# Optimization experiments

Measured on AMD Instinct MI355X. Metric: run time of the kernel, lower is better.

The kernel has to match this reference:

```python
import jax, jax.numpy as jnp
import numpy as np

N_NODES = 100000
N_EDGES = 1600000


def setup_inputs() -> dict:
    key = jax.random.key(0)
    ks = jax.random.split(key, 12)
    s = lambda d: 1.0 / np.sqrt(d)
    inp = {
        "x": jax.random.normal(ks[0], (N_NODES, 64), dtype=jnp.float32),
        "edge_index": jax.random.randint(ks[1], (2, N_EDGES), 0, N_NODES, dtype=jnp.int64),
        "W_embed": jax.random.normal(ks[2], (64, 128), dtype=jnp.float32) * s(64),
        "eps1": jnp.zeros((), jnp.float32),
        "w1a": jax.random.normal(ks[3], (128, 128), dtype=jnp.float32) * s(128),
        "b1a": jnp.zeros((128,), jnp.float32),
        "w1b": jax.random.normal(ks[4], (128, 128), dtype=jnp.float32) * s(128),
        "b1b": jnp.zeros((128,), jnp.float32),
        "eps2": jnp.zeros((), jnp.float32),
        "w2a": jax.random.normal(ks[5], (128, 256), dtype=jnp.float32) * s(128),
        "b2a": jnp.zeros((256,), jnp.float32),
        "w2b": jax.random.normal(ks[6], (256, 128), dtype=jnp.float32) * s(256),
        "b2b": jnp.zeros((128,), jnp.float32),
        "eps3": jnp.zeros((), jnp.float32),
        "w3a": jax.random.normal(ks[7], (128, 256), dtype=jnp.float32) * s(128),
        "b3a": jnp.zeros((256,), jnp.float32),
        "w3b": jax.random.normal(ks[8], (256, 128), dtype=jnp.float32) * s(256),
        "b3b": jnp.zeros((128,), jnp.float32),
    }
    return inp


def _aggregate(h, src, dst, n):
    # GINConv sum aggregation: out[i] = sum_{(j,i) in E} h[j]
    return jax.ops.segment_sum(h[src], dst, num_segments=n)


def reference(x, edge_index, W_embed, eps1, w1a, b1a, w1b, b1b,
              eps2, w2a, b2a, w2b, b2b, eps3, w3a, b3a, w3b, b3b):
    src, dst = edge_index[0], edge_index[1]
    n = x.shape[0]
    # node_attr_encoder: linear embedding (dropout p=0 -> identity)
    h = x @ W_embed  # [N, dim]
    # conv1: nn((1+eps)*h + sum_neighbors), nn = Lin->ReLU->Lin
    z = (1.0 + eps1) * h + _aggregate(h, src, dst, n)
    h = jax.nn.relu(z @ w1a + b1a) @ w1b + b1b
    # conv2/conv3: nn = Lin->ReLU->Lin->ReLU
    z = (1.0 + eps2) * h + _aggregate(h, src, dst, n)
    h = jax.nn.relu(jax.nn.relu(z @ w2a + b2a) @ w2b + b2b)
    z = (1.0 + eps3) * h + _aggregate(h, src, dst, n)
    h = jax.nn.relu(jax.nn.relu(z @ w3a + b3a) @ w3b + b3b)
    return h
```

## Files before the change

kernel.cpp:

```cpp
#include <hip/hip_runtime.h>
#include <hip/hip_bf16.h>
#include <stdint.h>


typedef __attribute__((ext_vector_type(8))) short short8;
typedef __attribute__((ext_vector_type(16))) float float16v;

#define BKT 512
#define NBMAX 256

__device__ __forceinline__ float b2f_lo(unsigned int u) {
    return __uint_as_float(u << 16);
}
__device__ __forceinline__ float b2f_hi(unsigned int u) {
    return __uint_as_float(u & 0xffff0000u);
}
__device__ __forceinline__ unsigned short f2b(float f) {
    unsigned int u = __float_as_uint(f);
    return (unsigned short)((u + 0x7fffu + ((u >> 16) & 1u)) >> 16);
}

__global__ void detect_i64_kernel(const unsigned int* ei, int* flag) {
    if (threadIdx.x == 0) {
        int is64 = 1;
        for (int e = 0; e < 64; ++e)
            if (ei[2 * e + 1] != 0u) { is64 = 0; break; }
        *flag = is64;
    }
}

__device__ __forceinline__ int edge_at(const int* ei32, int is64, long long pos) {
    if (is64) return (int)(((const long long*)ei32)[pos]);
    return ei32[pos];
}

__global__ __launch_bounds__(256) void part_hist_kernel(
        const int* __restrict__ ei, const int* __restrict__ flag,
        int* __restrict__ bh, int E, int NB, int PB) {
    __shared__ int h[NBMAX];
    const int g = blockIdx.x, tid = threadIdx.x;
    const int is64 = *flag;
    for (int i = tid; i < NB; i += 256) h[i] = 0;
    __syncthreads();
    const int e0 = g * PB, e1 = min(e0 + PB, E);
    for (int e = e0 + tid; e < e1; e += 256) {
        int d = edge_at(ei, is64, (long long)E + e);
        atomicAdd(&h[d >> 9], 1);
    }
    __syncthreads();
    for (int i = tid; i < NB; i += 256) bh[i * gridDim.x + g] = h[i];
}

__global__ __launch_bounds__(1024) void scan1_kernel(
        const int* __restrict__ in, int* __restrict__ out,
        int* __restrict__ partial, int n) {
    __shared__ int sm[1024];
    const int t = threadIdx.x;
    const int i = blockIdx.x * 1024 + t;
    int v = (i < n) ? in[i] : 0;
    sm[t] = v;
    __syncthreads();
#pragma unroll
    for (int off = 1; off < 1024; off <<= 1) {
        int x = (t >= off) ? sm[t - off] : 0;
        __syncthreads();
        sm[t] += x;
        __syncthreads();
    }
    if (i < n) out[i] = sm[t] - v;
    if (t == 1023) partial[blockIdx.x] = sm[1023];
}

__global__ __launch_bounds__(256) void scan2_kernel(
        int* __restrict__ partial, int* __restrict__ blockoff, int g1) {
    __shared__ int sm[256];
    const int t = threadIdx.x;
    int v = (t < g1) ? partial[t] : 0;
    sm[t] = v;
    __syncthreads();
#pragma unroll
    for (int off = 1; off < 256; off <<= 1) {
        int x = (t >= off) ? sm[t - off] : 0;
        __syncthreads();
        sm[t] += x;
        __syncthreads();
    }
    blockoff[t] = sm[t] - v;
}

__global__ __launch_bounds__(1024) void scan3g_kernel(
        int* __restrict__ a, const int* __restrict__ blockoff, int n) {
    int i = blockIdx.x * 1024 + threadIdx.x;
    if (i < n) a[i] += blockoff[blockIdx.x];
}

__global__ __launch_bounds__(256) void part_scatter_kernel(
        const int* __restrict__ ei, const int* __restrict__ flag,
        const int* __restrict__ bhs, unsigned int* __restrict__ staged,
        int E, int NB, int PB) {
    __shared__ int cur[NBMAX];
    const int g = blockIdx.x, tid = threadIdx.x;
    const int is64 = *flag;
    for (int i = tid; i < NB; i += 256) cur[i] = bhs[i * gridDim.x + g];
    __syncthreads();
    const int e0 = g * PB, e1 = min(e0 + PB, E);
    for (int e = e0 + tid; e < e1; e += 256) {
        int d = edge_at(ei, is64, (long long)E + e);
        int s = edge_at(ei, is64, (long long)e);
        int b = d >> 9;
        int p = atomicAdd(&cur[b], 1);
        staged[p] = ((unsigned int)(d & (BKT - 1)) << 17) | (unsigned int)s;
    }
}

__global__ __launch_bounds__(256) void csr_local_kernel(
        const unsigned int* __restrict__ staged, const int* __restrict__ bhs,
        int* __restrict__ offs, int* __restrict__ csr, int N, int E, int NB, int G2) {
    __shared__ int hist[BKT];
    __shared__ int cur[BKT];
    const int b = blockIdx.x;
    const int tid = threadIdx.x;
    const int start = bhs[b * G2];
    const int end = (b + 1 < NB) ? bhs[(b + 1) * G2] : E;
    const int node0 = b * BKT;
    for (int i = tid; i < BKT; i += 256) hist[i] = 0;
    __syncthreads();
    for (int i = start + tid; i < end; i += 256)
        atomicAdd(&hist[staged[i] >> 17], 1);
    __syncthreads();
    const int i0 = tid * 2, i1 = i0 + 1;
    for (int off = 1; off < BKT; off <<= 1) {
        int v0 = (i0 >= off) ? hist[i0 - off] : 0;
        int v1 = (i1 >= off) ? hist[i1 - off] : 0;
        __syncthreads();
        hist[i0] += v0;
        hist[i1] += v1;
        __syncthreads();
    }
    for (int i = tid; i < BKT; i += 256) {
        int node = node0 + i;
        if (node < N) {
            int e0 = start + ((i == 0) ? 0 : hist[i - 1]);
            offs[node] = e0;
            cur[i] = e0;
        }
    }
    if (b == NB - 1 && tid == 0) offs[N] = E;
    __syncthreads();
    for (int i = start + tid; i < end; i += 256) {
        unsigned int v = staged[i];
        int dl = v >> 17;
        int src = (int)(v & 0x1ffff);
        int p = atomicAdd(&cur[dl], 1);
        csr[p] = src;
    }
}

struct PW { const float* W; unsigned short* o; int K; int KOUT; };
struct PWAll { PW d[7]; int cum[8]; };

__global__ __launch_bounds__(256) void packall_kernel(PWAll P) {
    int id = blockIdx.x * blockDim.x + threadIdx.x;
    if (id >= P.cum[7]) return;
    int w = 0;
#pragma unroll
    for (int k = 1; k < 7; ++k) w += (id >= P.cum[k]);
    const int local = id - P.cum[w];
    const float* W = P.d[w].W;
    unsigned short* out = P.d[w].o;
    const int K = P.d[w].K, KOUT = P.d[w].KOUT;
    const int KS = K / 16;
    const int l = local & 63;
    const int s = (local >> 6) % KS;
    const int T = local / (KS * 64);
    const int kbase = s * 16 + ((l >> 5) << 3);
    const int n = T * 32 + (l & 31);
#pragma unroll
    for (int j = 0; j < 8; ++j)
        out[(long long)local * 8 + j] = f2b(W[(long long)(kbase + j) * KOUT + n]);
}

__global__ __launch_bounds__(256) void mm_embed(
        const float* __restrict__ X, const unsigned short* __restrict__ Wp,
        unsigned short* __restrict__ out, int Mreal) {
    constexpr int KS = 4;
    const int tid = threadIdx.x;
    const int w = tid >> 6;
    const int l = tid & 63;
    const int lm = l & 31;
    const int lk = l >> 5;
    const int wr = w & 1, wc = w >> 1;
    const long long R0 = (long long)blockIdx.x * 128 + wr * 64;
    const int T0 = (wc * 64) >> 5;

    const long long r0 = (R0 + lm < Mreal) ? (R0 + lm) : (Mreal - 1);
    const long long r1 = (R0 + 32 + lm < Mreal) ? (R0 + 32 + lm) : (Mreal - 1);
    const float* xr0 = X + r0 * 64 + lk * 8;
    const float* xr1 = X + r1 * 64 + lk * 8;
    const unsigned short* bb0 = Wp + ((long long)T0 * KS * 64 + l) * 8;
    const unsigned short* bb1 = Wp + ((long long)(T0 + 1) * KS * 64 + l) * 8;

    float16v acc00 = {}, acc01 = {}, acc10 = {}, acc11 = {};
#pragma unroll
    for (int s = 0; s < KS; ++s) {
        float4 f0a = *(const float4*)(xr0 + s * 16);
        float4 f0b = *(const float4*)(xr0 + s * 16 + 4);
        float4 f1a = *(const float4*)(xr1 + s * 16);
        float4 f1b = *(const float4*)(xr1 + s * 16 + 4);
        short8 a0, a1;
        a0[0] = (short)f2b(f0a.x); a0[1] = (short)f2b(f0a.y);
        a0[2] = (short)f2b(f0a.z); a0[3] = (short)f2b(f0a.w);
        a0[4] = (short)f2b(f0b.x); a0[5] = (short)f2b(f0b.y);
        a0[6] = (short)f2b(f0b.z); a0[7] = (short)f2b(f0b.w);
        a1[0] = (short)f2b(f1a.x); a1[1] = (short)f2b(f1a.y);
        a1[2] = (short)f2b(f1a.z); a1[3] = (short)f2b(f1a.w);
        a1[4] = (short)f2b(f1b.x); a1[5] = (short)f2b(f1b.y);
        a1[6] = (short)f2b(f1b.z); a1[7] = (short)f2b(f1b.w);
        short8 b0 = *(const short8*)(bb0 + (long long)s * 64 * 8);
        short8 b1 = *(const short8*)(bb1 + (long long)s * 64 * 8);
        acc00 = __builtin_amdgcn_mfma_f32_32x32x16_bf16(a0, b0, acc00, 0, 0, 0);
        acc01 = __builtin_amdgcn_mfma_f32_32x32x16_bf16(a0, b1, acc01, 0, 0, 0);
        acc10 = __builtin_amdgcn_mfma_f32_32x32x16_bf16(a1, b0, acc10, 0, 0, 0);
        acc11 = __builtin_amdgcn_mfma_f32_32x32x16_bf16(a1, b1, acc11, 0, 0, 0);
    }
    auto st = [&](float16v acc, long long rb, int col) {
#pragma unroll
        for (int r = 0; r < 16; ++r) {
            long long row = rb + (r & 3) + 8 * (r >> 2);
            out[row * 128 + col] = f2b(acc[r]);
        }
    };
    const long long rbase = R0 + 4 * lk;
    st(acc00, rbase,      wc * 64 + lm);
    st(acc01, rbase,      wc * 64 + 32 + lm);
    st(acc10, rbase + 32, wc * 64 + lm);
    st(acc11, rbase + 32, wc * 64 + 32 + lm);
}

__global__ __launch_bounds__(256) void aggz_kernel(
        const unsigned short* __restrict__ H, const int* __restrict__ offs,
        const int* __restrict__ csr, const float* __restrict__ eps,
        unsigned short* __restrict__ Z, int n) {
    const int node = blockIdx.x * 16 + (threadIdx.x >> 4);
    const int c8 = (threadIdx.x & 15) << 3;
    if (node >= n) return;
    const int beg = offs[node];
    const int end = offs[node + 1];
    float a0 = 0.f, a1 = 0.f, a2 = 0.f, a3 = 0.f;
    float a4 = 0.f, a5 = 0.f, a6 = 0.f, a7 = 0.f;
    int i = beg;
    for (; i + 3 < end; i += 4) {
        const int j0 = csr[i], j1 = csr[i + 1], j2 = csr[i + 2], j3 = csr[i + 3];
        const uint4 u0 = *(const uint4*)(H + ((long long)j0 << 7) + c8);
        const uint4 u1 = *(const uint4*)(H + ((long long)j1 << 7) + c8);
        const uint4 u2 = *(const uint4*)(H + ((long long)j2 << 7) + c8);
        const uint4 u3 = *(const uint4*)(H + ((long long)j3 << 7) + c8);
        a0 += (b2f_lo(u0.x) + b2f_lo(u1.x)) + (b2f_lo(u2.x) + b2f_lo(u3.x));
        a1 += (b2f_hi(u0.x) + b2f_hi(u1.x)) + (b2f_hi(u2.x) + b2f_hi(u3.x));
        a2 += (b2f_lo(u0.y) + b2f_lo(u1.y)) + (b2f_lo(u2.y) + b2f_lo(u3.y));
        a3 += (b2f_hi(u0.y) + b2f_hi(u1.y)) + (b2f_hi(u2.y) + b2f_hi(u3.y));
        a4 += (b2f_lo(u0.z) + b2f_lo(u1.z)) + (b2f_lo(u2.z) + b2f_lo(u3.z));
        a5 += (b2f_hi(u0.z) + b2f_hi(u1.z)) + (b2f_hi(u2.z) + b2f_hi(u3.z));
        a6 += (b2f_lo(u0.w) + b2f_lo(u1.w)) + (b2f_lo(u2.w) + b2f_lo(u3.w));
        a7 += (b2f_hi(u0.w) + b2f_hi(u1.w)) + (b2f_hi(u2.w) + b2f_hi(u3.w));
    }
    for (; i < end; ++i) {
        const uint4 u0 = *(const uint4*)(H + ((long long)csr[i] << 7) + c8);
        a0 += b2f_lo(u0.x); a1 += b2f_hi(u0.x);
        a2 += b2f_lo(u0.y); a3 += b2f_hi(u0.y);
        a4 += b2f_lo(u0.z); a5 += b2f_hi(u0.z);
        a6 += b2f_lo(u0.w); a7 += b2f_hi(u0.w);
    }
    const uint4 uh = *(const uint4*)(H + ((long long)node << 7) + c8);
    const float e = 1.0f + eps[0];
    a0 = fmaf(e, b2f_lo(uh.x), a0); a1 = fmaf(e, b2f_hi(uh.x), a1);
    a2 = fmaf(e, b2f_lo(uh.y), a2); a3 = fmaf(e, b2f_hi(uh.y), a3);
    a4 = fmaf(e, b2f_lo(uh.z), a4); a5 = fmaf(e, b2f_hi(uh.z), a5);
    a6 = fmaf(e, b2f_lo(uh.w), a6); a7 = fmaf(e, b2f_hi(uh.w), a7);
    uint4 o;
    o.x = ((unsigned int)f2b(a1) << 16) | (unsigned int)f2b(a0);
    o.y = ((unsigned int)f2b(a3) << 16) | (unsigned int)f2b(a2);
    o.z = ((unsigned int)f2b(a5) << 16) | (unsigned int)f2b(a4);
    o.w = ((unsigned int)f2b(a7) << 16) | (unsigned int)f2b(a6);
    *(uint4*)(Z + ((long long)node << 7) + c8) = o;
}

template<int KMID, bool RELU2, bool OUTF32>
__global__ __launch_bounds__(512) void fused_mlp(
        const unsigned short* __restrict__ Zin,
        const unsigned short* __restrict__ Wap, const float* __restrict__ ba,
        const unsigned short* __restrict__ Wbp, const float* __restrict__ bb,
        void* __restrict__ outp, int Mreal, int ntiles) {
    __shared__ unsigned short lds[16384];
    const int tid = threadIdx.x;
    const int w = tid >> 6;
    const int l = tid & 63;
    const int lm = l & 31;
    const int lk = l >> 5;
    const int wr = w & 1;
    const int wc = w >> 1;
    constexpr int KS1 = 8;
    constexpr int KSB = KMID / 16;
    constexpr int NH = KMID / 128;

    for (int tile = blockIdx.x; tile < ntiles; tile += gridDim.x) {
        const long long R0 = (long long)tile * 128;
        const unsigned short* arow0 = Zin + (R0 + wr * 64 + lm) * 128 + lk * 8;
        const unsigned short* arow1 = arow0 + 32 * 128;

        float16v d0 = {}, d1 = {};

        for (int h = 0; h < NH; ++h) {
            __syncthreads();

            {
                float16v c0 = {}, c1 = {};
                const int T1 = h * 4 + wc;
                const unsigned short* bp = Wap + ((long long)T1 * KS1 * 64 + l) * 8;
#pragma unroll
                for (int s = 0; s < KS1; ++s) {
                    short8 a0 = *(const short8*)(arow0 + s * 16);
                    short8 a1 = *(const short8*)(arow1 + s * 16);
                    short8 b = *(const short8*)(bp + (long long)s * 64 * 8);
                    c0 = __builtin_amdgcn_mfma_f32_32x32x16_bf16(a0, b, c0, 0, 0, 0);
                    c1 = __builtin_amdgcn_mfma_f32_32x32x16_bf16(a1, b, c1, 0, 0, 0);
                }
                auto wT = [&](float16v acc, int rbase, int cl) {
                    const float bv = ba[h * 128 + cl];
                    const int secT = cl >> 3;
                    const int cj = cl & 7;
#pragma unroll
                    for (int r = 0; r < 16; ++r) {
                        float v = fmaxf(acc[r] + bv, 0.f);
                        const int row = rbase + (r & 3) + 8 * (r >> 2);
                        lds[(secT * 128 + (row ^ (secT & 7))) * 8 + cj] = f2b(v);
                    }
                };
                wT(c0, wr * 64 + 4 * lk,      wc * 32 + lm);
                wT(c1, wr * 64 + 32 + 4 * lk, wc * 32 + lm);
            }
            __syncthreads();

            {
                const unsigned short* bp = Wbp + ((long long)wc * KSB * 64 + l) * 8;
#pragma unroll
                for (int s = 0; s < 8; ++s) {
                    const int sec = s * 2 + lk;
                    short8 a0 = *(const short8*)&lds[(sec * 128 + ((wr * 64 + lm) ^ (sec & 7))) * 8];
                    short8 a1 = *(const short8*)&lds[(sec * 128 + ((wr * 64 + 32 + lm) ^ (sec & 7))) * 8];
                    short8 b = *(const short8*)(bp + (long long)(h * 8 + s) * 64 * 8);
                    d0 = __builtin_amdgcn_mfma_f32_32x32x16_bf16(a0, b, d0, 0, 0, 0);
                    d1 = __builtin_amdgcn_mfma_f32_32x32x16_bf16(a1, b, d1, 0, 0, 0);
                }
            }
        }

        auto st = [&](float16v acc, int rbase, int col) {
            const float bv = bb[col];
#pragma unroll
            for (int r = 0; r < 16; ++r) {
                float v = acc[r] + bv;
                if (RELU2) v = fmaxf(v, 0.f);
                const long long row = R0 + rbase + (r & 3) + 8 * (r >> 2);
                if (OUTF32) {
                    if (row < Mreal) ((float*)outp)[row * 128 + col] = v;
                } else {
                    ((unsigned short*)outp)[row * 128 + col] = f2b(v);
                }
            }
        };
        st(d0, wr * 64 + 4 * lk,      wc * 32 + lm);
        st(d1, wr * 64 + 32 + 4 * lk, wc * 32 + lm);
    }
}

extern "C" void kernel_launch(void* const* d_in, const int* in_sizes, int n_in,
                              void* d_out, int out_size, void* d_ws, size_t ws_size,
                              hipStream_t stream) {
    const float* x    = (const float*)d_in[0];
    const int*   ei   = (const int*)d_in[1];
    const float* Wemb = (const float*)d_in[2];
    const float* eps1 = (const float*)d_in[3];
    const float* w1a  = (const float*)d_in[4];
    const float* b1a  = (const float*)d_in[5];
    const float* w1b  = (const float*)d_in[6];
    const float* b1b  = (const float*)d_in[7];
    const float* eps2 = (const float*)d_in[8];
    const float* w2a  = (const float*)d_in[9];
    const float* b2a  = (const float*)d_in[10];
    const float* w2b  = (const float*)d_in[11];
    const float* b2b  = (const float*)d_in[12];
    const float* eps3 = (const float*)d_in[13];
    const float* w3a  = (const float*)d_in[14];
    const float* b3a  = (const float*)d_in[15];
    const float* w3b  = (const float*)d_in[16];
    const float* b3b  = (const float*)d_in[17];

    const int N = in_sizes[0] / 64;
    const int E = in_sizes[1] / 2;
    const int Mpad = ((N + 127) / 128) * 128;
    const int NB = (N + BKT - 1) / BKT;
    const int G2 = 1024;
    const int PB = (E + G2 - 1) / G2;
    const int BH = NB * G2;

    char* ws = (char*)d_ws;
    size_t off = 0;
    auto alloc = [&](size_t bytes) -> void* {
        void* p = ws + off;
        off = (off + bytes + 255) & ~(size_t)255;
        return p;
    };
    unsigned short* Ha  = (unsigned short*)alloc((size_t)Mpad * 128 * 2);
    unsigned short* Hb2 = (unsigned short*)alloc((size_t)Mpad * 128 * 2);
    unsigned short* Zb  = (unsigned short*)alloc((size_t)Mpad * 128 * 2);
    unsigned short* pWe = (unsigned short*)alloc((size_t)64 * 128 * 2);
    unsigned short* p1a = (unsigned short*)alloc((size_t)128 * 128 * 2);
    unsigned short* p1b = (unsigned short*)alloc((size_t)128 * 128 * 2);
    unsigned short* p2a = (unsigned short*)alloc((size_t)128 * 256 * 2);
    unsigned short* p2b = (unsigned short*)alloc((size_t)256 * 128 * 2);
    unsigned short* p3a = (unsigned short*)alloc((size_t)128 * 256 * 2);
    unsigned short* p3b = (unsigned short*)alloc((size_t)256 * 128 * 2);
    int* offs = (int*)alloc((size_t)(N + 1) * 4);
    int* csr  = (int*)alloc((size_t)E * 4);
    unsigned int* staged = (unsigned int*)alloc((size_t)E * 4);
    int* bh   = (int*)alloc((size_t)BH * 4);
    int* bhs  = (int*)alloc((size_t)BH * 4);
    int* part = (int*)alloc(1024);
    int* boff = (int*)alloc(1024);
    int* flag = (int*)alloc(256);

    detect_i64_kernel<<<1, 64, 0, stream>>>((const unsigned int*)ei, flag);
    part_hist_kernel<<<G2, 256, 0, stream>>>(ei, flag, bh, E, NB, PB);
    const int G1 = (BH + 1023) / 1024;
    scan1_kernel<<<G1, 1024, 0, stream>>>(bh, bhs, part, BH);
    scan2_kernel<<<1, 256, 0, stream>>>(part, boff, G1);
    scan3g_kernel<<<G1, 1024, 0, stream>>>(bhs, boff, BH);
    part_scatter_kernel<<<G2, 256, 0, stream>>>(ei, flag, bhs, staged, E, NB, PB);
    csr_local_kernel<<<NB, 256, 0, stream>>>(staged, bhs, offs, csr, N, E, NB, G2);

    {
        PWAll P;
        const PW descs[7] = {
            {Wemb, pWe, 64, 128}, {w1a, p1a, 128, 128}, {w1b, p1b, 128, 128},
            {w2a, p2a, 128, 256}, {w2b, p2b, 256, 128}, {w3a, p3a, 128, 256},
            {w3b, p3b, 256, 128}};
        int c = 0;
        for (int k = 0; k < 7; ++k) {
            P.d[k] = descs[k];
            P.cum[k] = c;
            c += (descs[k].KOUT / 32) * (descs[k].K / 16) * 64;
        }
        P.cum[7] = c;
        packall_kernel<<<(c + 255) / 256, 256, 0, stream>>>(P);
    }

    const int MMB = Mpad / 128;
    const int AGB = (N + 15) / 16;
    const int PGRID = 512;

    mm_embed<<<MMB, 256, 0, stream>>>(x, pWe, Ha, N);

    aggz_kernel<<<AGB, 256, 0, stream>>>(Ha, offs, csr, eps1, Zb, N);
    fused_mlp<128, false, false><<<PGRID, 512, 0, stream>>>(Zb, p1a, b1a, p1b, b1b, Hb2, N, MMB);

    aggz_kernel<<<AGB, 256, 0, stream>>>(Hb2, offs, csr, eps2, Zb, N);
    fused_mlp<256, true, false><<<PGRID, 512, 0, stream>>>(Zb, p2a, b2a, p2b, b2b, Ha, N, MMB);

    aggz_kernel<<<AGB, 256, 0, stream>>>(Ha, offs, csr, eps3, Zb, N);
    fused_mlp<256, true, true><<<PGRID, 512, 0, stream>>>(Zb, p3a, b3a, p3b, b3b, d_out, N, MMB);
}
```

Before: 490.3 us.

## Rewrite fused MLP as per-wave register-resident strips without LDS round-trip

Replaces the 128-row block-tiled fused MLP, which staged the hidden activations through LDS with barriers, with a kernel in which each wave owns a 32-node strip. The first GEMM is computed transposed (weights as the A operand, Z as B) so the accumulator can be converted to bf16 with v_cvt_pk_bf16_f32 and rearranged with v_permlane32_swap directly into A-operand registers for the second GEMM. This removes LDS traffic and __syncthreads, and folds the first bias into the accumulator initialisation. In exchange it uses many more registers (whole hidden row held in registers), re-reads weights from global or cache once per wave, and launches one block per four strips instead of a persistent grid.

```diff
diff --git a/kernel.cpp b/kernel.cpp
--- a/kernel.cpp
+++ b/kernel.cpp
@@ -5,9 +5,14 @@
 
 typedef __attribute__((ext_vector_type(8))) short short8;
 typedef __attribute__((ext_vector_type(16))) float float16v;
+typedef __attribute__((ext_vector_type(4))) unsigned int uint4v;
 
 #define BKT 512
 #define NBMAX 256
+
+#define MFMA32 __builtin_amdgcn_mfma_f32_32x32x16_bf16
+
+union U4S8 { uint4v u; short8 s; };
 
 __device__ __forceinline__ float b2f_lo(unsigned int u) {
     return __uint_as_float(u << 16);
@@ -18,6 +23,14 @@
 __device__ __forceinline__ unsigned short f2b(float f) {
     unsigned int u = __float_as_uint(f);
     return (unsigned short)((u + 0x7fffu + ((u >> 16) & 1u)) >> 16);
+}
+__device__ __forceinline__ unsigned cvtpk_bf16(float a, float b) {
+    unsigned r;
+    asm("v_cvt_pk_bf16_f32 %0, %1, %2" : "=v"(r) : "v"(a), "v"(b));
+    return r;
+}
+__device__ __forceinline__ void perm32swap(unsigned& a, unsigned& b) {
+    asm("v_permlane32_swap_b32 %0, %1" : "+v"(a), "+v"(b));
 }
 
 __global__ void detect_i64_kernel(const unsigned int* ei, int* flag) {
@@ -218,10 +231,10 @@
         a1[6] = (short)f2b(f1b.z); a1[7] = (short)f2b(f1b.w);
         short8 b0 = *(const short8*)(bb0 + (long long)s * 64 * 8);
         short8 b1 = *(const short8*)(bb1 + (long long)s * 64 * 8);
-        acc00 = __builtin_amdgcn_mfma_f32_32x32x16_bf16(a0, b0, acc00, 0, 0, 0);
-        acc01 = __builtin_amdgcn_mfma_f32_32x32x16_bf16(a0, b1, acc01, 0, 0, 0);
-        acc10 = __builtin_amdgcn_mfma_f32_32x32x16_bf16(a1, b0, acc10, 0, 0, 0);
-        acc11 = __builtin_amdgcn_mfma_f32_32x32x16_bf16(a1, b1, acc11, 0, 0, 0);
+        acc00 = MFMA32(a0, b0, acc00, 0, 0, 0);
+        acc01 = MFMA32(a0, b1, acc01, 0, 0, 0);
+        acc10 = MFMA32(a1, b0, acc10, 0, 0, 0);
+        acc11 = MFMA32(a1, b1, acc11, 0, 0, 0);
     }
     auto st = [&](float16v acc, long long rb, int col) {
 #pragma unroll
@@ -285,92 +298,105 @@
     *(uint4*)(Z + ((long long)node << 7) + c8) = o;
 }
 
+
+#define CVT_TO_PA(ACC, CBASE) do {                                     \
+        unsigned X1 = cvtpk_bf16((ACC)[0], (ACC)[1]);                  \
+        unsigned Y1 = cvtpk_bf16((ACC)[4], (ACC)[5]);                  \
+        unsigned X2 = cvtpk_bf16((ACC)[2], (ACC)[3]);                  \
+        unsigned Y2 = cvtpk_bf16((ACC)[6], (ACC)[7]);                  \
+        perm32swap(X1, Y1); perm32swap(X2, Y2);                        \
+        U4S8 u0; u0.u[0] = X1; u0.u[1] = X2; u0.u[2] = Y1; u0.u[3] = Y2; \
+        pa[(CBASE)] = u0.s;                                            \
+        unsigned X3 = cvtpk_bf16((ACC)[8], (ACC)[9]);                  \
+        unsigned Y3 = cvtpk_bf16((ACC)[12], (ACC)[13]);                \
+        unsigned X4 = cvtpk_bf16((ACC)[10], (ACC)[11]);                \
+        unsigned Y4 = cvtpk_bf16((ACC)[14], (ACC)[15]);                \
+        perm32swap(X3, Y3); perm32swap(X4, Y4);                        \
+        U4S8 u1; u1.u[0] = X3; u1.u[1] = X4; u1.u[2] = Y3; u1.u[3] = Y4; \
+        pa[(CBASE) + 1] = u1.s;                                        \
+    } while (0)
+
 template<int KMID, bool RELU2, bool OUTF32>
-__global__ __launch_bounds__(512) void fused_mlp(
+__global__ __launch_bounds__(256, 2) void fused_mlp2(
         const unsigned short* __restrict__ Zin,
         const unsigned short* __restrict__ Wap, const float* __restrict__ ba,
         const unsigned short* __restrict__ Wbp, const float* __restrict__ bb,
-        void* __restrict__ outp, int Mreal, int ntiles) {
-    __shared__ unsigned short lds[16384];
+        void* __restrict__ outp, int Mreal, int nstrips) {
+    constexpr int NF = KMID / 32;
+    constexpr int NCH = KMID / 16;
     const int tid = threadIdx.x;
-    const int w = tid >> 6;
+    const int wid = tid >> 6;
     const int l = tid & 63;
-    const int lm = l & 31;
-    const int lk = l >> 5;
-    const int wr = w & 1;
-    const int wc = w >> 1;
-    constexpr int KS1 = 8;
-    constexpr int KSB = KMID / 16;
-    constexpr int NH = KMID / 128;
-
-    for (int tile = blockIdx.x; tile < ntiles; tile += gridDim.x) {
-        const long long R0 = (long long)tile * 128;
-        const unsigned short* arow0 = Zin + (R0 + wr * 64 + lm) * 128 + lk * 8;
-        const unsigned short* arow1 = arow0 + 32 * 128;
-
-        float16v d0 = {}, d1 = {};
-
-        for (int h = 0; h < NH; ++h) {
-            __syncthreads();
-
-            {
-                float16v c0 = {}, c1 = {};
-                const int T1 = h * 4 + wc;
-                const unsigned short* bp = Wap + ((long long)T1 * KS1 * 64 + l) * 8;
-#pragma unroll
-                for (int s = 0; s < KS1; ++s) {
-                    short8 a0 = *(const short8*)(arow0 + s * 16);
-                    short8 a1 = *(const short8*)(arow1 + s * 16);
-                    short8 b = *(const short8*)(bp + (long long)s * 64 * 8);
-                    c0 = __builtin_amdgcn_mfma_f32_32x32x16_bf16(a0, b, c0, 0, 0, 0);
-                    c1 = __builtin_amdgcn_mfma_f32_32x32x16_bf16(a1, b, c1, 0, 0, 0);
-                }
-                auto wT = [&](float16v acc, int rbase, int cl) {
-                    const float bv = ba[h * 128 + cl];
-                    const int secT = cl >> 3;
-                    const int cj = cl & 7;
-#pragma unroll
-                    for (int r = 0; r < 16; ++r) {
-                        float v = fmaxf(acc[r] + bv, 0.f);
-                        const int row = rbase + (r & 3) + 8 * (r >> 2);
-                        lds[(secT * 128 + (row ^ (secT & 7))) * 8 + cj] = f2b(v);
-                    }
-                };
-                wT(c0, wr * 64 + 4 * lk,      wc * 32 + lm);
-                wT(c1, wr * 64 + 32 + 4 * lk, wc * 32 + lm);
+    const int lo = l & 31;
+    const int hi = l >> 5;
+    const int strip = blockIdx.x * 4 + wid;
+    if (strip >= nstrips) return;
+    const long long node0 = (long long)strip * 32;
+
+    long long zr = node0 + lo;
+    if (zr >= Mreal) zr = Mreal - 1;
+    const unsigned short* zrow = Zin + zr * 128 + hi * 8;
+    short8 z[8];
+#pragma unroll
+    for (int s = 0; s < 8; ++s) z[s] = *(const short8*)(zrow + s * 16);
+
+    short8 pa[NCH];
+
+#pragma unroll
+    for (int fp = 0; fp < NF / 2; ++fp) {
+        const int f0 = 2 * fp, f1 = 2 * fp + 1;
+        float16v accA, accB;
+#pragma unroll
+        for (int q = 0; q < 4; ++q) {
+            const float4 tA = *(const float4*)(ba + f0 * 32 + q * 8 + hi * 4);
+            const float4 tB = *(const float4*)(ba + f1 * 32 + q * 8 + hi * 4);
+            accA[4 * q + 0] = tA.x; accA[4 * q + 1] = tA.y;
+            accA[4 * q + 2] = tA.z; accA[4 * q + 3] = tA.w;
+            accB[4 * q + 0] = tB.x; accB[4 * q + 1] = tB.y;
+            accB[4 * q + 2] = tB.z; accB[4 * q + 3] = tB.w;
+        }
+        const unsigned short* wa0 = Wap + ((long long)f0 * 8 * 64 + l) * 8;
+        const unsigned short* wa1 = Wap + ((long long)f1 * 8 * 64 + l) * 8;
+#pragma unroll
+        for (int s = 0; s < 8; ++s) {
+            short8 a0 = *(const short8*)(wa0 + (long long)s * 64 * 8);
+            short8 a1 = *(const short8*)(wa1 + (long long)s * 64 * 8);
+            accA = MFMA32(a0, z[s], accA, 0, 0, 0);
+            accB = MFMA32(a1, z[s], accB, 0, 0, 0);
+        }
+#pragma unroll
+        for (int r = 0; r < 16; ++r) {
+            accA[r] = fmaxf(accA[r], 0.f);
+            accB[r] = fmaxf(accB[r], 0.f);
+        }
+        CVT_TO_PA(accA, 4 * fp);
+        CVT_TO_PA(accB, 4 * fp + 2);
+    }
+
+    float16v acc2[4] = {};
+#pragma unroll
+    for (int c = 0; c < NCH; ++c) {
+#pragma unroll
+        for (int g = 0; g < 4; ++g) {
+            short8 b = *(const short8*)(Wbp + ((long long)(g * NCH + c) * 64 + l) * 8);
+            acc2[g] = MFMA32(pa[c], b, acc2[g], 0, 0, 0);
+        }
+    }
+
+#pragma unroll
+    for (int g = 0; g < 4; ++g) {
+        const int col = g * 32 + lo;
+        const float bv = bb[col];
+#pragma unroll
+        for (int r = 0; r < 16; ++r) {
+            float v = acc2[g][r] + bv;
+            if (RELU2) v = fmaxf(v, 0.f);
+            const long long node = node0 + (r & 3) + 8 * (r >> 2) + 4 * hi;
+            if (node < Mreal) {
+                if (OUTF32) ((float*)outp)[node * 128 + col] = v;
+                else ((unsigned short*)outp)[node * 128 + col] = f2b(v);
             }
-            __syncthreads();
-
-            {
-                const unsigned short* bp = Wbp + ((long long)wc * KSB * 64 + l) * 8;
-#pragma unroll
-                for (int s = 0; s < 8; ++s) {
-                    const int sec = s * 2 + lk;
-                    short8 a0 = *(const short8*)&lds[(sec * 128 + ((wr * 64 + lm) ^ (sec & 7))) * 8];
-                    short8 a1 = *(const short8*)&lds[(sec * 128 + ((wr * 64 + 32 + lm) ^ (sec & 7))) * 8];
-                    short8 b = *(const short8*)(bp + (long long)(h * 8 + s) * 64 * 8);
-                    d0 = __builtin_amdgcn_mfma_f32_32x32x16_bf16(a0, b, d0, 0, 0, 0);
-                    d1 = __builtin_amdgcn_mfma_f32_32x32x16_bf16(a1, b, d1, 0, 0, 0);
-                }
-            }
-        }
-
-        auto st = [&](float16v acc, int rbase, int col) {
-            const float bv = bb[col];
-#pragma unroll
-            for (int r = 0; r < 16; ++r) {
-                float v = acc[r] + bv;
-                if (RELU2) v = fmaxf(v, 0.f);
-                const long long row = R0 + rbase + (r & 3) + 8 * (r >> 2);
-                if (OUTF32) {
-                    if (row < Mreal) ((float*)outp)[row * 128 + col] = v;
-                } else {
-                    ((unsigned short*)outp)[row * 128 + col] = f2b(v);
-                }
-            }
-        };
-        st(d0, wr * 64 + 4 * lk,      wc * 32 + lm);
-        st(d1, wr * 64 + 32 + 4 * lk, wc * 32 + lm);
+        }
     }
 }
 
@@ -457,16 +483,17 @@
 
     const int MMB = Mpad / 128;
     const int AGB = (N + 15) / 16;
-    const int PGRID = 512;
+    const int NSTRIP = (N + 31) / 32;
+    const int MLPB = (NSTRIP + 3) / 4;
 
     mm_embed<<<MMB, 256, 0, stream>>>(x, pWe, Ha, N);
 
     aggz_kernel<<<AGB, 256, 0, stream>>>(Ha, offs, csr, eps1, Zb, N);
-    fused_mlp<128, false, false><<<PGRID, 512, 0, stream>>>(Zb, p1a, b1a, p1b, b1b, Hb2, N, MMB);
+    fused_mlp2<128, false, false><<<MLPB, 256, 0, stream>>>(Zb, p1a, b1a, p1b, b1b, Hb2, N, NSTRIP);
 
     aggz_kernel<<<AGB, 256, 0, stream>>>(Hb2, offs, csr, eps2, Zb, N);
-    fused_mlp<256, true, false><<<PGRID, 512, 0, stream>>>(Zb, p2a, b2a, p2b, b2b, Ha, N, MMB);
+    fused_mlp2<256, true, false><<<MLPB, 256, 0, stream>>>(Zb, p2a, b2a, p2b, b2b, Ha, N, NSTRIP);
 
     aggz_kernel<<<AGB, 256, 0, stream>>>(Ha, offs, csr, eps3, Zb, N);
-    fused_mlp<256, true, true><<<PGRID, 512, 0, stream>>>(Zb, p3a, b3a, p3b, b3b, d_out, N, MMB);
-}
+    fused_mlp2<256, true, true><<<MLPB, 256, 0, stream>>>(Zb, p3a, b3a, p3b, b3b, d_out, N, NSTRIP);
+}
```

Measured after the change: 517.1 us. 1.05x slower.
